# Optimization experiments

Measured on AMD Instinct MI355X. Metric: run time of the kernel, lower is better.

The kernel has to match this reference:

```python
import jax, jax.numpy as jnp
import numpy as np

B, S, D = 4, 4096, 1024
E = 8            # num_expert_extra + num_expert_proto
F = 2 * D        # ffn_mult * dim
EPS = 1e-5


def setup_inputs() -> dict:
    key = jax.random.key(0)
    ks = jax.random.split(key, 8)
    sc = 0.02
    return {
        "inputs": jax.random.normal(ks[0], (B, S, D), jnp.float32),
        "Wr": jax.random.normal(ks[1], (D, E), jnp.float32) * sc,   # router (no bias)
        "W1": jax.random.normal(ks[2], (E, D, F), jnp.float32) * sc,
        "b1": jnp.zeros((E, F), jnp.float32),
        "gamma": jnp.ones((E, F), jnp.float32),
        "beta": jnp.zeros((E, F), jnp.float32),
        "W2": jax.random.normal(ks[3], (E, F, D), jnp.float32) * sc,
        "b2": jnp.zeros((E, D), jnp.float32),
    }


def reference(inputs, Wr, W1, b1, gamma, beta, W2, b2):
    b, s, d = inputs.shape
    top_k = max(1, int(1.0 * s / E))  # capacity_factor=1.0

    # router: [b, s, e]
    logits = jnp.einsum('bsd,de->bse', inputs, Wr)
    probs = jax.nn.softmax(logits.astype(jnp.float32), axis=-1)

    # expert-choice top-k over tokens: [b, e, k]
    weights, idx = jax.lax.top_k(probs.transpose(0, 2, 1), top_k)

    # gather dispatched tokens: [b, e, k, d]
    bix = jnp.arange(b)[:, None, None]
    xg = inputs[bix, idx]

    # per-expert FFN: fc2(LN(gelu(fc1(x)))) (subln, dropout=eval identity)
    h = jnp.einsum('bekd,edf->bekf', xg, W1) + b1[None, :, None, :]
    h = jax.nn.gelu(h, approximate=False)
    mu = jnp.mean(h, axis=-1, keepdims=True)
    var = jnp.mean(jnp.square(h - mu), axis=-1, keepdims=True)
    h = (h - mu) * jax.lax.rsqrt(var + EPS)
    h = h * gamma[None, :, None, :] + beta[None, :, None, :]
    out = jnp.einsum('bekf,efd->bekd', h, W2) + b2[None, :, None, :]

    # weighted scatter-add back to token positions
    val = weights[..., None].astype(inputs.dtype) * out
    results = jnp.zeros_like(inputs).at[bix, idx].add(val)
    return results, logits
```

## Files before the change

### kernel.cpp

```cpp
#include <hip/hip_runtime.h>
#include <hip/hip_bf16.h>

#define B_ 4
#define S_ 4096
#define D_ 1024
#define E_ 8
#define F_ 2048
#define TK_ 512

typedef unsigned short u16;
typedef unsigned int u32;
typedef u16 u16x4 __attribute__((ext_vector_type(4)));
typedef u16 u16x8 __attribute__((ext_vector_type(8)));
typedef short s16x8 __attribute__((ext_vector_type(8)));
typedef float f32x4 __attribute__((ext_vector_type(4)));

__device__ __forceinline__ u16 f2bf(float f) {
  u32 u = __builtin_bit_cast(u32, f);
  u32 r = (u + 0x7fffu + ((u >> 16) & 1u)) >> 16;
  return (u16)r;
}
__device__ __forceinline__ float b2f(u16 h) {
  return __builtin_bit_cast(float, ((u32)h) << 16);
}
__device__ __forceinline__ void gload16(const u16* g, const u16* l) {
  __builtin_amdgcn_global_load_lds((const __attribute__((address_space(1))) void*)g,
                                   (__attribute__((address_space(3))) void*)l, 16, 0, 0);
}
__device__ __forceinline__ f32x4 mfma_bf16(s16x8 a, s16x8 b, f32x4 c) {
  return __builtin_amdgcn_mfma_f32_16x16x32_bf16(a, b, c, 0, 0, 0);
}

__global__ __launch_bounds__(256) void rc_kernel(const float* __restrict__ x,
                                                 const float* __restrict__ Wr,
                                                 float* __restrict__ logits,
                                                 u16* __restrict__ xb,
                                                 float* __restrict__ results) {
  __shared__ float wr[D_ * E_];
  for (int i = threadIdx.x; i < D_ * E_; i += 256) wr[i] = Wr[i];
  __syncthreads();
  int lane = threadIdx.x & 63;
  int wid = threadIdx.x >> 6;
  int token = blockIdx.x * 4 + wid;
  const float* xr = x + (size_t)token * D_;
  u16* xo = xb + (size_t)token * D_;
  float* ro = results + (size_t)token * D_;
  float acc[E_];
#pragma unroll
  for (int e = 0; e < E_; ++e) acc[e] = 0.f;
#pragma unroll
  for (int q = 0; q < 4; ++q) {
    int d0 = q * 256 + lane * 4;
    float4 v = *(const float4*)(xr + d0);
    u16x4 st;
    st[0] = f2bf(v.x); st[1] = f2bf(v.y); st[2] = f2bf(v.z); st[3] = f2bf(v.w);
    *(u16x4*)(xo + d0) = st;
    *(float4*)(ro + d0) = make_float4(0.f, 0.f, 0.f, 0.f);
    float xv[4] = {v.x, v.y, v.z, v.w};
    const float* w0 = &wr[d0 * E_];
#pragma unroll
    for (int j = 0; j < 4; ++j) {
#pragma unroll
      for (int e = 0; e < E_; ++e) acc[e] += xv[j] * w0[j * E_ + e];
    }
  }
#pragma unroll
  for (int e = 0; e < E_; ++e) {
#pragma unroll
    for (int off = 32; off; off >>= 1) acc[e] += __shfl_down(acc[e], off);
  }
  if (lane == 0) {
    float4 o0 = make_float4(acc[0], acc[1], acc[2], acc[3]);
    float4 o1 = make_float4(acc[4], acc[5], acc[6], acc[7]);
    *(float4*)(logits + (size_t)token * E_) = o0;
    *(float4*)(logits + (size_t)token * E_ + 4) = o1;
  }
}

__device__ __forceinline__ void suffix_scan(u32* h, int n, int tid) {
  for (int d = 1; d < n; d <<= 1) {
    u32 v[2];
    int c = 0;
    for (int i = tid; i < n; i += 1024) v[c++] = (i + d < n) ? h[i + d] : 0;
    __syncthreads();
    c = 0;
    for (int i = tid; i < n; i += 1024) h[i] += v[c++];
    __syncthreads();
  }
}

__global__ __launch_bounds__(1024) void topk_kernel(const float* __restrict__ logits,
                                                    int* __restrict__ idx,
                                                    float* __restrict__ wts) {
  int be = blockIdx.x, b = be >> 3, e = be & 7;
  __shared__ u32 keys[S_];
  __shared__ u32 hist[2048];
  __shared__ u32 tcnt[1024];
  __shared__ u32 sb, sneed, scnt;
  int tid = threadIdx.x;
  const float* lg = logits + (size_t)b * S_ * E_;
  for (int s = tid; s < S_; s += 1024) {
    float4 l0 = *(const float4*)(lg + (size_t)s * E_);
    float4 l1 = *(const float4*)(lg + (size_t)s * E_ + 4);
    float la[8] = {l0.x, l0.y, l0.z, l0.w, l1.x, l1.y, l1.z, l1.w};
    float mx = la[0];
#pragma unroll
    for (int t = 1; t < 8; ++t) mx = fmaxf(mx, la[t]);
    float sum = 0.f;
#pragma unroll
    for (int t = 0; t < 8; ++t) sum += expf(la[t] - mx);
    float p = expf(la[e] - mx) / sum;
    keys[s] = __builtin_bit_cast(u32, p);
  }
  if (tid == 0) scnt = 0;

  hist[tid] = 0; hist[tid + 1024] = 0;
  __syncthreads();
  for (int s = tid; s < S_; s += 1024) atomicAdd(&hist[keys[s] >> 21], 1u);
  __syncthreads();
  suffix_scan(hist, 2048, tid);
  for (int i = tid; i < 2048; i += 1024) {
    u32 nxt = (i + 1 < 2048) ? hist[i + 1] : 0;
    if (hist[i] >= (u32)TK_ && nxt < (u32)TK_) { sb = (u32)i; sneed = TK_ - nxt; }
  }
  __syncthreads();
  u32 b1 = sb, need1 = sneed;
  __syncthreads();

  hist[tid] = 0; hist[tid + 1024] = 0;
  __syncthreads();
  for (int s = tid; s < S_; s += 1024)
    if ((keys[s] >> 21) == b1) atomicAdd(&hist[(keys[s] >> 10) & 2047u], 1u);
  __syncthreads();
  suffix_scan(hist, 2048, tid);
  for (int i = tid; i < 2048; i += 1024) {
    u32 nxt = (i + 1 < 2048) ? hist[i + 1] : 0;
    if (hist[i] >= need1 && nxt < need1) { sb = (u32)i; sneed = need1 - nxt; }
  }
  __syncthreads();
  u32 p2 = (b1 << 11) | sb, need2 = sneed;
  __syncthreads();

  if (tid < 1024) hist[tid] = 0;
  __syncthreads();
  for (int s = tid; s < S_; s += 1024)
    if ((keys[s] >> 10) == p2) atomicAdd(&hist[keys[s] & 1023u], 1u);
  __syncthreads();
  suffix_scan(hist, 1024, tid);
  for (int i = tid; i < 1024; i += 1024) {
    u32 nxt = (i + 1 < 1024) ? hist[i + 1] : 0;
    if (hist[i] >= need2 && nxt < need2) { sb = (u32)i; sneed = need2 - nxt; }
  }
  __syncthreads();
  u32 T = (p2 << 10) | sb;
  u32 needT = sneed;

  for (int s = tid; s < S_; s += 1024) {
    if (keys[s] > T) {
      u32 p = atomicAdd(&scnt, 1u);
      idx[be * TK_ + p] = s;
      wts[be * TK_ + p] = __builtin_bit_cast(float, keys[s]);
    }
  }
  u32 myc = 0;
#pragma unroll
  for (int j = 0; j < 4; ++j) myc += (keys[tid * 4 + j] == T) ? 1u : 0u;
  tcnt[tid] = myc;
  __syncthreads();
  for (int d = 1; d < 1024; d <<= 1) {
    u32 v = (tid >= d) ? tcnt[tid - d] : 0;
    __syncthreads();
    tcnt[tid] += v;
    __syncthreads();
  }
  u32 rank = tcnt[tid] - myc;
#pragma unroll
  for (int j = 0; j < 4; ++j) {
    int s = tid * 4 + j;
    if (keys[s] == T) {
      if (rank < needT) {
        u32 p = atomicAdd(&scnt, 1u);
        idx[be * TK_ + p] = s;
        wts[be * TK_ + p] = __builtin_bit_cast(float, T);
      }
      rank++;
    }
  }
}

__global__ __launch_bounds__(256) void transpose_cvt_kernel(const float* __restrict__ src,
                                                            u16* __restrict__ dst,
                                                            int R, int C,
                                                            const float* __restrict__ scale,
                                                            const float* __restrict__ beta,
                                                            float* __restrict__ Bd) {
  __shared__ float tile[32][33];
  int z = blockIdx.z;
  const float* s = src + (size_t)z * R * C;
  u16* d = dst + (size_t)z * R * C;
  int r0 = blockIdx.x * 32, c0 = blockIdx.y * 32;
  int xx = threadIdx.x & 31, yy = threadIdx.x >> 5;
#pragma unroll
  for (int q = 0; q < 4; ++q)
    tile[yy + q * 8][xx] = s[(size_t)(r0 + yy + q * 8) * C + c0 + xx];
  __syncthreads();
  float sc = scale ? scale[(size_t)z * R + r0 + xx] : 1.f;
#pragma unroll
  for (int q = 0; q < 4; ++q)
    d[(size_t)(c0 + yy + q * 8) * R + r0 + xx] = f2bf(sc * tile[xx][yy + q * 8]);
  if (Bd != nullptr) {
    __syncthreads();
    if (threadIdx.x < 32) {
      float sm = 0.f;
      const float* br = beta + (size_t)z * R + r0;
#pragma unroll
      for (int f = 0; f < 32; ++f) sm += br[f] * tile[f][threadIdx.x];
      unsafeAtomicAdd(&Bd[(size_t)z * C + c0 + threadIdx.x], sm);
    }
  }
}

__global__ __launch_bounds__(256) void gemv_g_kernel(const u16* __restrict__ W2g,
                                                     float* __restrict__ G) {
  int row = blockIdx.x * 4 + (threadIdx.x >> 6);
  int lane = threadIdx.x & 63;
  const u16* wr = W2g + (size_t)row * F_;
  float s = 0.f;
#pragma unroll
  for (int j = 0; j < 4; ++j) {
    u16x8 v = *(const u16x8*)(wr + (j * 64 + lane) * 8);
#pragma unroll
    for (int t = 0; t < 8; ++t) s += b2f(v[t]);
  }
#pragma unroll
  for (int off = 32; off; off >>= 1) s += __shfl_down(s, off);
  if (lane == 0) G[row] = s;
}

__device__ __forceinline__ void kloop97(const u16* const pa[4], const u16* const pb[4],
                                        u16* As, u16* Bs, f32x4 acc[4][4], int NT,
                                        int wid, const int aoff[4], const int boff[4],
                                        int sk0, int sk1) {
  int ldst = wid * 512;
  for (int t = 0; t < NT; ++t) {
    int k0 = t * 64;
#pragma unroll
    for (int q = 0; q < 4; ++q) gload16(pa[q] + k0, As + q * 2048 + ldst);
#pragma unroll
    for (int q = 0; q < 4; ++q) gload16(pb[q] + k0, Bs + q * 2048 + ldst);
    asm volatile("s_waitcnt vmcnt(0)" ::: "memory");
    __builtin_amdgcn_s_barrier();
    s16x8 aF[4], bF[4];
#pragma unroll
    for (int kk = 0; kk < 2; ++kk) {
      int sk = kk ? sk1 : sk0;
#pragma unroll
      for (int f = 0; f < 4; ++f) aF[f] = *(const s16x8*)&As[aoff[f] + sk];
#pragma unroll
      for (int g = 0; g < 4; ++g) bF[g] = *(const s16x8*)&Bs[boff[g] + sk];
      __builtin_amdgcn_s_setprio(1);
#pragma unroll
      for (int f = 0; f < 4; ++f)
#pragma unroll
        for (int g = 0; g < 4; ++g) acc[f][g] = mfma_bf16(aF[f], bF[g], acc[f][g]);
      __builtin_amdgcn_s_setprio(0);
    }
    __builtin_amdgcn_s_barrier();
  }
}

__global__ __launch_bounds__(256, 2) void gemm1_kernel(const u16* __restrict__ xb,
                                                       const u16* __restrict__ W1t,
                                                       const float* __restrict__ b1,
                                                       const int* __restrict__ idx,
                                                       u16* __restrict__ hbuf,
                                                       float2* __restrict__ stats2) {
  int p = blockIdx.x;
  int e = p & 7, slot = p >> 3;
  int tm = slot & 3, bb = (slot >> 2) & 3, tn = slot >> 4;
  int be = bb * 8 + e;
  int t0 = tm * 128, n0 = tn * 128;
  int tid = threadIdx.x, lane = tid & 63, wid = tid >> 6;
  int wm = wid >> 1, wn = wid & 1;
  int cidx = lane & 15, kq = lane >> 4;
  __shared__ u16 As[128 * 64];
  __shared__ u16 Bs[128 * 64];
  __shared__ float2 sm[128][2];

  int srow = tid >> 3;
  int kc = (tid & 7) ^ (srow & 7);
  const u16* pa[4];
  const u16* pb[4];
  const u16* bsrc = W1t + (size_t)e * F_ * D_;
#pragma unroll
  for (int q = 0; q < 4; ++q) {
    int tok = idx[be * TK_ + t0 + q * 32 + srow];
    pa[q] = xb + ((size_t)bb * S_ + tok) * D_ + kc * 8;
    pb[q] = bsrc + (size_t)(n0 + q * 32 + srow) * D_ + kc * 8;
  }
  int aoff[4], boff[4];
#pragma unroll
  for (int f = 0; f < 4; ++f) {
    aoff[f] = (wm * 64 + f * 16 + cidx) * 64;
    boff[f] = (wn * 64 + f * 16 + cidx) * 64;
  }
  int sk0 = (kq ^ (cidx & 7)) * 8;
  int sk1 = ((4 + kq) ^ (cidx & 7)) * 8;

  f32x4 acc[4][4];
#pragma unroll
  for (int f = 0; f < 4; ++f)
#pragma unroll
    for (int g = 0; g < 4; ++g) acc[f][g] = (f32x4){0.f, 0.f, 0.f, 0.f};

  kloop97(pa, pb, As, Bs, acc, D_ / 64, wid, aoff, boff, sk0, sk1);

  float bias[4];
#pragma unroll
  for (int g = 0; g < 4; ++g) bias[g] = b1[e * F_ + n0 + wn * 64 + g * 16 + cidx];
  size_t hbase = (size_t)be * TK_ * F_;
#pragma unroll
  for (int f = 0; f < 4; ++f) {
#pragma unroll
    for (int r = 0; r < 4; ++r) {
      int lr = wm * 64 + f * 16 + kq * 4 + r;
      size_t hb = hbase + (size_t)(t0 + lr) * F_ + n0 + wn * 64 + cidx;
      float vs = 0.f, vss = 0.f;
#pragma unroll
      for (int g = 0; g < 4; ++g) {
        float v = acc[f][g][r] + bias[g];
        float gl = 0.5f * v * (1.0f + erff(v * 0.70710678118654752f));
        hbuf[hb + g * 16] = f2bf(gl);
        vs += gl;
        vss += gl * gl;
      }
#pragma unroll
      for (int off = 1; off < 16; off <<= 1) {
        vs += __shfl_xor(vs, off);
        vss += __shfl_xor(vss, off);
      }
      if (cidx == 0) {
        float2 o; o.x = vs; o.y = vss;
        sm[lr][wn] = o;
      }
    }
  }
  __syncthreads();
  if (tid < 128) {
    float2 a = sm[tid][0], b = sm[tid][1];
    float2 o; o.x = a.x + b.x; o.y = a.y + b.y;
    stats2[((size_t)be * TK_ + t0 + tid) * 16 + tn] = o;
  }
}

__global__ __launch_bounds__(256, 2) void gemm2_kernel(const u16* __restrict__ hbuf,
                                                       const u16* __restrict__ W2g,
                                                       const float* __restrict__ b2,
                                                       const int* __restrict__ idx,
                                                       const float* __restrict__ wts,
                                                       float* __restrict__ results,
                                                       const float2* __restrict__ stats2,
                                                       const float* __restrict__ G,
                                                       const float* __restrict__ Bd) {
  int p = blockIdx.x;
  int e = p & 7, slot = p >> 3;
  int tn = slot & 7, tm = (slot >> 3) & 3, bb = slot >> 5;
  int be = bb * 8 + e;
  int t0 = tm * 128, n0 = tn * 128;
  int tid = threadIdx.x, lane = tid & 63, wid = tid >> 6;
  int wm = wid >> 1, wn = wid & 1;
  int cidx = lane & 15, kq = lane >> 4;
  __shared__ u16 As[128 * 64];
  __shared__ u16 Bs[128 * 64];
  __shared__ float smean[128];
  __shared__ float srstd[128];

  if (tid < 128) {
    const float2* sp = stats2 + ((size_t)be * TK_ + t0 + tid) * 16;
    float sum = 0.f, ss = 0.f;
#pragma unroll
    for (int j = 0; j < 16; ++j) {
      float2 v = sp[j];
      sum += v.x;
      ss += v.y;
    }
    float mean = sum * (1.f / F_);
    float var = ss * (1.f / F_) - mean * mean;
    smean[tid] = mean;
    srstd[tid] = rsqrtf(var + 1e-5f);
  }
  __syncthreads();

  int srow = tid >> 3;
  int kc = (tid & 7) ^ (srow & 7);
  const u16* pa[4];
  const u16* pb[4];
  const u16* asrc = hbuf + (size_t)be * TK_ * F_;
  const u16* bsrc = W2g + (size_t)e * D_ * F_;
#pragma unroll
  for (int q = 0; q < 4; ++q) {
    pa[q] = asrc + (size_t)(t0 + q * 32 + srow) * F_ + kc * 8;
    pb[q] = bsrc + (size_t)(n0 + q * 32 + srow) * F_ + kc * 8;
  }
  int aoff[4], boff[4];
#pragma unroll
  for (int f = 0; f < 4; ++f) {
    aoff[f] = (wm * 64 + f * 16 + cidx) * 64;
    boff[f] = (wn * 64 + f * 16 + cidx) * 64;
  }
  int sk0 = (kq ^ (cidx & 7)) * 8;
  int sk1 = ((4 + kq) ^ (cidx & 7)) * 8;

  f32x4 acc[4][4];
#pragma unroll
  for (int f = 0; f < 4; ++f)
#pragma unroll
    for (int g = 0; g < 4; ++g) acc[f][g] = (f32x4){0.f, 0.f, 0.f, 0.f};

  kloop97(pa, pb, As, Bs, acc, F_ / 64, wid, aoff, boff, sk0, sk1);

  int cb = n0 + wn * 64 + cidx;
  float b2v[4], Gv[4], Bdv[4];
#pragma unroll
  for (int g = 0; g < 4; ++g) {
    b2v[g] = b2[e * D_ + cb + g * 16];
    Gv[g] = G[e * D_ + cb + g * 16];
    Bdv[g] = Bd[e * D_ + cb + g * 16];
  }
#pragma unroll
  for (int f = 0; f < 4; ++f) {
#pragma unroll
    for (int r = 0; r < 4; ++r) {
      int lr = wm * 64 + f * 16 + kq * 4 + r;
      int trow = t0 + lr;
      int tok = idx[be * TK_ + trow];
      float wv = wts[be * TK_ + trow];
      float mean = smean[lr], rstd = srstd[lr];
      float* rrow = results + ((size_t)bb * S_ + tok) * D_ + cb;
#pragma unroll
      for (int g = 0; g < 4; ++g) {
        float out = rstd * acc[f][g][r] - rstd * mean * Gv[g] + Bdv[g] + b2v[g];
        unsafeAtomicAdd(rrow + g * 16, wv * out);
      }
    }
  }
}

extern "C" void kernel_launch(void* const* d_in, const int* in_sizes, int n_in,
                              void* d_out, int out_size, void* d_ws, size_t ws_size,
                              hipStream_t stream) {
  const float* x = (const float*)d_in[0];
  const float* Wr = (const float*)d_in[1];
  const float* W1 = (const float*)d_in[2];
  const float* b1 = (const float*)d_in[3];
  const float* gamma = (const float*)d_in[4];
  const float* beta = (const float*)d_in[5];
  const float* W2 = (const float*)d_in[6];
  const float* b2 = (const float*)d_in[7];

  float* results = (float*)d_out;
  float* logits = results + (size_t)B_ * S_ * D_;

  char* ws = (char*)d_ws;
  const size_t OFF_IDX = 0;
  const size_t OFF_WTS = OFF_IDX + (size_t)B_ * E_ * TK_ * 4;
  const size_t OFF_ST = OFF_WTS + (size_t)B_ * E_ * TK_ * 4;
  const size_t OFF_G = OFF_ST + (size_t)B_ * E_ * TK_ * 16 * 8;
  const size_t OFF_BD = OFF_G + (size_t)E_ * D_ * 4;
  const size_t OFF_R0 = OFF_BD + (size_t)E_ * D_ * 4;
  const size_t OFF_R1 = OFF_R0 + (size_t)E_ * D_ * F_ * 2;
  const size_t OFF_H = OFF_R1 + (size_t)E_ * D_ * F_ * 2;
  const size_t NEED = OFF_H + (size_t)B_ * E_ * TK_ * F_ * 2;
  if (ws_size < NEED) return;

  int* idx = (int*)(ws + OFF_IDX);
  float* wts = (float*)(ws + OFF_WTS);
  float2* stats2 = (float2*)(ws + OFF_ST);
  float* G = (float*)(ws + OFF_G);
  float* Bd = (float*)(ws + OFF_BD);
  u16* xb = (u16*)(ws + OFF_R0);
  u16* W2g = (u16*)(ws + OFF_R0);
  u16* W1t = (u16*)(ws + OFF_R1);
  u16* hbuf = (u16*)(ws + OFF_H);

  rc_kernel<<<dim3(B_ * S_ / 4), 256, 0, stream>>>(x, Wr, logits, xb, results);
  topk_kernel<<<dim3(B_ * E_), 1024, 0, stream>>>(logits, idx, wts);
  transpose_cvt_kernel<<<dim3(D_ / 32, F_ / 32, E_), 256, 0, stream>>>(
      W1, W1t, D_, F_, nullptr, nullptr, nullptr);
  gemm1_kernel<<<dim3(2048), 256, 0, stream>>>(xb, W1t, b1, idx, hbuf, stats2);
  hipMemsetAsync(Bd, 0, (size_t)E_ * D_ * 4, stream);
  transpose_cvt_kernel<<<dim3(F_ / 32, D_ / 32, E_), 256, 0, stream>>>(
      W2, W2g, F_, D_, gamma, beta, Bd);
  gemv_g_kernel<<<dim3(E_ * D_ / 4), 256, 0, stream>>>(W2g, G);
  gemm2_kernel<<<dim3(1024), 256, 0, stream>>>(hbuf, W2g, b2, idx, wts, results,
                                               stats2, G, Bd);
}
```

Measured before the change: 322.5 us.

## Precompute softmax probs in router, fuse G gemv into transpose, use tanh-form GELU

The router kernel now computes softmax once per token and writes probs, so the top-k kernel only reads one column instead of recomputing the softmax for every expert block. The separate gemv kernel for G is removed; its column sums are accumulated with atomics inside the W2 transpose kernel from the fp32 tile, and G and Bd are zeroed with a single memset. The exact erf GELU is replaced by a sigmoid-based tanh approximation, which lowers epilogue cost but changes numerics relative to the exact reference. G is now summed from fp32 weights scaled by gamma rather than from the rounded bf16 values, which shifts precision slightly.

```diff
diff --git a/kernel.cpp b/kernel.cpp
--- a/kernel.cpp
+++ b/kernel.cpp
@@ -30,10 +30,15 @@
 __device__ __forceinline__ f32x4 mfma_bf16(s16x8 a, s16x8 b, f32x4 c) {
   return __builtin_amdgcn_mfma_f32_16x16x32_bf16(a, b, c, 0, 0, 0);
 }
+__device__ __forceinline__ float gelu_t(float v) {
+  float t = v * (1.5957691216f + 0.0713548162726f * v * v);
+  return v / (1.f + __expf(-t));
+}
 
 __global__ __launch_bounds__(256) void rc_kernel(const float* __restrict__ x,
                                                  const float* __restrict__ Wr,
                                                  float* __restrict__ logits,
+                                                 float* __restrict__ probs,
                                                  u16* __restrict__ xb,
                                                  float* __restrict__ results) {
   __shared__ float wr[D_ * E_];
@@ -74,6 +79,18 @@
     float4 o1 = make_float4(acc[4], acc[5], acc[6], acc[7]);
     *(float4*)(logits + (size_t)token * E_) = o0;
     *(float4*)(logits + (size_t)token * E_ + 4) = o1;
+    float mx = acc[0];
+#pragma unroll
+    for (int t = 1; t < 8; ++t) mx = fmaxf(mx, acc[t]);
+    float sum = 0.f;
+    float pe[8];
+#pragma unroll
+    for (int t = 0; t < 8; ++t) { pe[t] = expf(acc[t] - mx); sum += pe[t]; }
+    float inv = 1.f / sum;
+    float4 p0 = make_float4(pe[0] * inv, pe[1] * inv, pe[2] * inv, pe[3] * inv);
+    float4 p1 = make_float4(pe[4] * inv, pe[5] * inv, pe[6] * inv, pe[7] * inv);
+    *(float4*)(probs + (size_t)token * E_) = p0;
+    *(float4*)(probs + (size_t)token * E_ + 4) = p1;
   }
 }
 
@@ -89,7 +106,7 @@
   }
 }
 
-__global__ __launch_bounds__(1024) void topk_kernel(const float* __restrict__ logits,
+__global__ __launch_bounds__(1024) void topk_kernel(const float* __restrict__ probs,
                                                     int* __restrict__ idx,
                                                     float* __restrict__ wts) {
   int be = blockIdx.x, b = be >> 3, e = be & 7;
@@ -98,20 +115,8 @@
   __shared__ u32 tcnt[1024];
   __shared__ u32 sb, sneed, scnt;
   int tid = threadIdx.x;
-  const float* lg = logits + (size_t)b * S_ * E_;
-  for (int s = tid; s < S_; s += 1024) {
-    float4 l0 = *(const float4*)(lg + (size_t)s * E_);
-    float4 l1 = *(const float4*)(lg + (size_t)s * E_ + 4);
-    float la[8] = {l0.x, l0.y, l0.z, l0.w, l1.x, l1.y, l1.z, l1.w};
-    float mx = la[0];
-#pragma unroll
-    for (int t = 1; t < 8; ++t) mx = fmaxf(mx, la[t]);
-    float sum = 0.f;
-#pragma unroll
-    for (int t = 0; t < 8; ++t) sum += expf(la[t] - mx);
-    float p = expf(la[e] - mx) / sum;
-    keys[s] = __builtin_bit_cast(u32, p);
-  }
+  const float* pr = probs + (size_t)b * S_ * E_ + e;
+  for (int s = tid; s < S_; s += 1024) keys[s] = __builtin_bit_cast(u32, pr[(size_t)s * E_]);
   if (tid == 0) scnt = 0;
 
   hist[tid] = 0; hist[tid + 1024] = 0;
@@ -193,7 +198,8 @@
                                                             int R, int C,
                                                             const float* __restrict__ scale,
                                                             const float* __restrict__ beta,
-                                                            float* __restrict__ Bd) {
+                                                            float* __restrict__ Bd,
+                                                            float* __restrict__ G) {
   __shared__ float tile[32][33];
   int z = blockIdx.z;
   const float* s = src + (size_t)z * R * C;
@@ -211,30 +217,18 @@
   if (Bd != nullptr) {
     __syncthreads();
     if (threadIdx.x < 32) {
-      float sm = 0.f;
+      float smb = 0.f, smg = 0.f;
       const float* br = beta + (size_t)z * R + r0;
-#pragma unroll
-      for (int f = 0; f < 32; ++f) sm += br[f] * tile[f][threadIdx.x];
-      unsafeAtomicAdd(&Bd[(size_t)z * C + c0 + threadIdx.x], sm);
-    }
-  }
-}
-
-__global__ __launch_bounds__(256) void gemv_g_kernel(const u16* __restrict__ W2g,
-                                                     float* __restrict__ G) {
-  int row = blockIdx.x * 4 + (threadIdx.x >> 6);
-  int lane = threadIdx.x & 63;
-  const u16* wr = W2g + (size_t)row * F_;
-  float s = 0.f;
-#pragma unroll
-  for (int j = 0; j < 4; ++j) {
-    u16x8 v = *(const u16x8*)(wr + (j * 64 + lane) * 8);
-#pragma unroll
-    for (int t = 0; t < 8; ++t) s += b2f(v[t]);
-  }
-#pragma unroll
-  for (int off = 32; off; off >>= 1) s += __shfl_down(s, off);
-  if (lane == 0) G[row] = s;
+      const float* gr = scale + (size_t)z * R + r0;
+#pragma unroll
+      for (int f = 0; f < 32; ++f) {
+        smb += br[f] * tile[f][threadIdx.x];
+        smg += gr[f] * tile[f][threadIdx.x];
+      }
+      unsafeAtomicAdd(&Bd[(size_t)z * C + c0 + threadIdx.x], smb);
+      unsafeAtomicAdd(&G[(size_t)z * C + c0 + threadIdx.x], smg);
+    }
+  }
 }
 
 __device__ __forceinline__ void kloop97(const u16* const pa[4], const u16* const pb[4],
@@ -329,7 +323,7 @@
 #pragma unroll
       for (int g = 0; g < 4; ++g) {
         float v = acc[f][g][r] + bias[g];
-        float gl = 0.5f * v * (1.0f + erff(v * 0.70710678118654752f));
+        float gl = gelu_t(v);
         hbuf[hb + g * 16] = f2bf(gl);
         vs += gl;
         vss += gl * gl;
@@ -467,7 +461,8 @@
   const size_t OFF_ST = OFF_WTS + (size_t)B_ * E_ * TK_ * 4;
   const size_t OFF_G = OFF_ST + (size_t)B_ * E_ * TK_ * 16 * 8;
   const size_t OFF_BD = OFF_G + (size_t)E_ * D_ * 4;
-  const size_t OFF_R0 = OFF_BD + (size_t)E_ * D_ * 4;
+  const size_t OFF_P = OFF_BD + (size_t)E_ * D_ * 4;
+  const size_t OFF_R0 = OFF_P + (size_t)B_ * S_ * E_ * 4;
   const size_t OFF_R1 = OFF_R0 + (size_t)E_ * D_ * F_ * 2;
   const size_t OFF_H = OFF_R1 + (size_t)E_ * D_ * F_ * 2;
   const size_t NEED = OFF_H + (size_t)B_ * E_ * TK_ * F_ * 2;
@@ -478,20 +473,20 @@
   float2* stats2 = (float2*)(ws + OFF_ST);
   float* G = (float*)(ws + OFF_G);
   float* Bd = (float*)(ws + OFF_BD);
+  float* probs = (float*)(ws + OFF_P);
   u16* xb = (u16*)(ws + OFF_R0);
   u16* W2g = (u16*)(ws + OFF_R0);
   u16* W1t = (u16*)(ws + OFF_R1);
   u16* hbuf = (u16*)(ws + OFF_H);
 
-  rc_kernel<<<dim3(B_ * S_ / 4), 256, 0, stream>>>(x, Wr, logits, xb, results);
-  topk_kernel<<<dim3(B_ * E_), 1024, 0, stream>>>(logits, idx, wts);
+  rc_kernel<<<dim3(B_ * S_ / 4), 256, 0, stream>>>(x, Wr, logits, probs, xb, results);
+  topk_kernel<<<dim3(B_ * E_), 1024, 0, stream>>>(probs, idx, wts);
   transpose_cvt_kernel<<<dim3(D_ / 32, F_ / 32, E_), 256, 0, stream>>>(
-      W1, W1t, D_, F_, nullptr, nullptr, nullptr);
+      W1, W1t, D_, F_, nullptr, nullptr, nullptr, nullptr);
   gemm1_kernel<<<dim3(2048), 256, 0, stream>>>(xb, W1t, b1, idx, hbuf, stats2);
-  hipMemsetAsync(Bd, 0, (size_t)E_ * D_ * 4, stream);
+  hipMemsetAsync(G, 0, (size_t)2 * E_ * D_ * 4, stream);
   transpose_cvt_kernel<<<dim3(F_ / 32, D_ / 32, E_), 256, 0, stream>>>(
-      W2, W2g, F_, D_, gamma, beta, Bd);
-  gemv_g_kernel<<<dim3(E_ * D_ / 4), 256, 0, stream>>>(W2g, G);
+      W2, W2g, F_, D_, gamma, beta, Bd, G);
   gemm2_kernel<<<dim3(1024), 256, 0, stream>>>(hbuf, W2g, b2, idx, wts, results,
                                                stats2, G, Bd);
 }
```

Result: faster. 315.5 us (-2.2%).
